# Performance work log

Hardware: AMD Instinct MI355X
Metric: run time of the kernel (lower is better)

## Reference

```python
import jax, jax.numpy as jnp
import numpy as np

N = 768
D = 2
MARGIN = 0.01


def setup_inputs() -> dict:
    key = jax.random.key(0)
    k1, _ = jax.random.split(key)
    node_pos = jax.random.normal(k1, (N, D), dtype=jnp.float32)
    batch = jnp.zeros((N,), dtype=jnp.int32)  # unused by the loss math
    return {"node_pos": node_pos, "batch": batch}


def reference(node_pos, batch):
    n = node_pos.shape[0]
    # all unordered node pairs (equivalent to torch.combinations(arange(n), r=2))
    i_idx, j_idx = jnp.triu_indices(n, k=1)
    pi = node_pos[i_idx]              # [m, d]
    pj = node_pos[j_idx]              # [m, d]
    midpoints = 0.5 * (pi + pj)       # [m, d]
    radii = 0.5 * jnp.linalg.norm(pi - pj, axis=1) + MARGIN  # [m]
    # Euclidean cdist(node_pos [n,d], midpoints [m,d]) via expanded quadratic form
    x_sq = jnp.sum(node_pos * node_pos, axis=1)          # [n]
    m_sq = jnp.sum(midpoints * midpoints, axis=1)        # [m]
    cross = node_pos @ midpoints.T                       # [n, m]
    dist_sq = x_sq[:, None] + m_sq[None, :] - 2.0 * cross
    distances = jnp.sqrt(jnp.maximum(dist_sq, 0.0))      # [n, m]
    energy = jnp.square(jax.nn.relu(radii[None, :] - distances))
    return jnp.mean(energy)
```

## Files before the change

kernel.cpp:

```cpp
#include <hip/hip_runtime.h>

#define NN 768
#define NPAIRS ((NN * (NN - 1)) / 2)
#define MARGIN_F 0.01f

__global__ void gg_zero(float* out) { *out = 0.0f; }

__global__ __launch_bounds__(256) void gg_main(const float* __restrict__ pos,
                                               float* __restrict__ out,
                                               float inv_total) {
    int p = blockIdx.x * blockDim.x + threadIdx.x;
    float acc = 0.0f;

    if (p < NPAIRS) {
        const float A = 2.0f * NN - 1.0f;
        float disc = A * A - 8.0f * (float)p;
        int i = (int)((A - __builtin_amdgcn_sqrtf(disc)) * 0.5f);
        if (i < 0) i = 0;
        if (i > NN - 2) i = NN - 2;
        while (((i + 1) * (2 * NN - 1 - (i + 1))) / 2 <= p) ++i;
        while ((i * (2 * NN - 1 - i)) / 2 > p) --i;
        int off = (i * (2 * NN - 1 - i)) / 2;
        int j = i + 1 + (p - off);

        float xix = pos[2 * i], xiy = pos[2 * i + 1];
        float xjx = pos[2 * j], xjy = pos[2 * j + 1];
        float mx = 0.5f * (xix + xjx);
        float my = 0.5f * (xiy + xjy);
        float ddx = xix - xjx, ddy = xiy - xjy;
        float r = 0.5f * __builtin_amdgcn_sqrtf(fmaf(ddx, ddx, ddy * ddy)) + MARGIN_F;

        #pragma unroll 8
        for (int k = 0; k < NN; ++k) {
            float dx = pos[2 * k]     - mx;
            float dy = pos[2 * k + 1] - my;
            float d2 = fmaf(dx, dx, dy * dy);
            float d  = __builtin_amdgcn_sqrtf(d2);
            float t  = fmaxf(r - d, 0.0f);
            acc = fmaf(t, t, acc);
        }
    }

    for (int o = 32; o > 0; o >>= 1) acc += __shfl_down(acc, o);

    __shared__ float ws[4];
    int lane = threadIdx.x & 63;
    int wid  = threadIdx.x >> 6;
    if (lane == 0) ws[wid] = acc;
    __syncthreads();
    if (threadIdx.x == 0) {
        float s = (ws[0] + ws[1]) + (ws[2] + ws[3]);
        atomicAdd(out, s * inv_total);
    }
}

extern "C" void kernel_launch(void* const* d_in, const int* in_sizes, int n_in,
                              void* d_out, int out_size, void* d_ws, size_t ws_size,
                              hipStream_t stream) {
    const float* pos = (const float*)d_in[0];
    float* out = (float*)d_out;

    gg_zero<<<1, 1, 0, stream>>>(out);

    double total = (double)NN * (double)NPAIRS;
    float inv_total = (float)(1.0 / total);

    int blocks = (NPAIRS + 255) / 256;
    gg_main<<<blocks, 256, 0, stream>>>(pos, out, inv_total);
}
```

Measured before the change: 113.7 us.

## Precompute node norms, use expanded distance form, split node loop across grid

A small pre-kernel packs each node as a float4 of (x, y, x²+y²). The inner loop then computes squared distance through the expanded quadratic form, with one vector load per node. The node loop is also split into three chunks along gridDim.y to add parallelism, and the zero kernel is replaced by a memset. There is no clamp of negative d2 before the sqrt, so cancellation could produce NaN, and the split triples the number of atomic adds.

```diff
diff --git a/kernel.cpp b/kernel.cpp
--- a/kernel.cpp
+++ b/kernel.cpp
@@ -3,13 +3,24 @@
 #define NN 768
 #define NPAIRS ((NN * (NN - 1)) / 2)
 #define MARGIN_F 0.01f
+#define CHUNK 256
+#define NCHUNK 3
 
-__global__ void gg_zero(float* out) { *out = 0.0f; }
+__global__ __launch_bounds__(256) void gg_pre(const float* __restrict__ pos,
+                                              float4* __restrict__ nd) {
+    int i = blockIdx.x * blockDim.x + threadIdx.x;
+    if (i < NN) {
+        float x = pos[2 * i], y = pos[2 * i + 1];
+        nd[i] = make_float4(x, y, fmaf(x, x, y * y), 0.0f);
+    }
+}
 
 __global__ __launch_bounds__(256) void gg_main(const float* __restrict__ pos,
+                                               const float4* __restrict__ nd,
                                                float* __restrict__ out,
                                                float inv_total) {
     int p = blockIdx.x * blockDim.x + threadIdx.x;
+    int kbase = blockIdx.y * CHUNK;
     float acc = 0.0f;
 
     if (p < NPAIRS) {
@@ -28,13 +39,16 @@
         float mx = 0.5f * (xix + xjx);
         float my = 0.5f * (xiy + xjy);
         float ddx = xix - xjx, ddy = xiy - xjy;
-        float r = 0.5f * __builtin_amdgcn_sqrtf(fmaf(ddx, ddx, ddy * ddy)) + MARGIN_F;
+        float r  = 0.5f * __builtin_amdgcn_sqrtf(fmaf(ddx, ddx, ddy * ddy)) + MARGIN_F;
+        float cx = -2.0f * mx;
+        float cy = -2.0f * my;
+        float cc = fmaf(mx, mx, my * my);
 
         #pragma unroll 8
-        for (int k = 0; k < NN; ++k) {
-            float dx = pos[2 * k]     - mx;
-            float dy = pos[2 * k + 1] - my;
-            float d2 = fmaf(dx, dx, dy * dy);
+        for (int k = kbase; k < kbase + CHUNK; ++k) {
+            float4 n = nd[k];
+            float c  = cc + n.z;
+            float d2 = fmaf(n.x, cx, fmaf(n.y, cy, c));
             float d  = __builtin_amdgcn_sqrtf(d2);
             float t  = fmaxf(r - d, 0.0f);
             acc = fmaf(t, t, acc);
@@ -59,12 +73,14 @@
                               hipStream_t stream) {
     const float* pos = (const float*)d_in[0];
     float* out = (float*)d_out;
+    float4* nd = (float4*)d_ws;
 
-    gg_zero<<<1, 1, 0, stream>>>(out);
+    hipMemsetAsync(out, 0, sizeof(float), stream);
+    gg_pre<<<NCHUNK, 256, 0, stream>>>(pos, nd);
 
     double total = (double)NN * (double)NPAIRS;
     float inv_total = (float)(1.0 / total);
 
-    int blocks = (NPAIRS + 255) / 256;
-    gg_main<<<blocks, 256, 0, stream>>>(pos, out, inv_total);
+    dim3 grid((NPAIRS + 255) / 256, NCHUNK);
+    gg_main<<<grid, 256, 0, stream>>>(pos, nd, out, inv_total);
 }
```

Result: faster. 111.1 us (-2.3%).
